# Kernel tuning notes

Measured on AMD Instinct MI355X. Metric: run time of the kernel, lower is better.

The kernel has to match this reference:

```python
import jax, jax.numpy as jnp
import numpy as np

K = 3      # kernel size
P = 1      # padding
HEADS = 6  # num_heads


def setup_inputs() -> dict:
    key = jax.random.key(0)
    ks = jax.random.split(key, 6)
    B, H, W, C = 2, 48, 48, 192
    kk4h = K ** 4 * HEADS  # 486
    sc = 0.02
    return {
        "x": jax.random.normal(ks[0], (B, H, W, C), jnp.float32),
        "v_w": jax.random.normal(ks[1], (C, C), jnp.float32) * sc,
        "attn_w": jax.random.normal(ks[2], (kk4h, C), jnp.float32) * sc,
        "attn_b": jax.random.normal(ks[3], (kk4h,), jnp.float32) * sc,
        "proj_w": jax.random.normal(ks[4], (C, C), jnp.float32) * sc,
        "proj_b": jax.random.normal(ks[5], (C,), jnp.float32) * sc,
    }


def reference(x, v_w, attn_w, attn_b, proj_w, proj_b):
    # OutlookAttention with k=3, s=1 (pool is identity, h=H, w=W), p=1
    B, H, W, C = x.shape
    hd = C // HEADS
    scale = float(hd) ** -0.5

    # value projection (Linear, no bias): [B,H,W,C]
    v = x @ v_w.T

    # unfold: gather kxk neighborhood per pixel, row-major kernel order
    vp = jnp.pad(v, ((0, 0), (P, P), (P, P), (0, 0)))
    patches = jnp.stack(
        [vp[:, ki:ki + H, kj:kj + W, :] for ki in range(K) for kj in range(K)],
        axis=3,
    )  # [B,H,W,k*k,C]
    # -> [B, heads, hw, k*k, hd]
    v_ = patches.reshape(B, H * W, K * K, HEADS, hd).transpose(0, 3, 1, 2, 4)

    # attention logits from (pooled == identity) x: [B,H,W,k^4*heads]
    a = x @ attn_w.T + attn_b
    a = a.reshape(B, H * W, HEADS, K * K, K * K).transpose(0, 2, 1, 3, 4)
    a = jax.nn.softmax(a * scale, axis=-1)  # [B,heads,hw,kk,kk]

    # windowed attention
    out = jnp.einsum("bnlij,bnljd->bnlid", a, v_)  # [B,heads,hw,kk,hd]

    # fold (col2im): scatter-add each kernel tap back, then crop padding
    o = out.transpose(0, 2, 3, 1, 4).reshape(B, H, W, K * K, C)
    acc = jnp.zeros((B, H + 2 * P, W + 2 * P, C), dtype=o.dtype)
    idx = 0
    for ki in range(K):
        for kj in range(K):
            acc = acc.at[:, ki:ki + H, kj:kj + W, :].add(o[:, :, :, idx, :])
            idx += 1
    folded = acc[:, P:P + H, P:P + W, :]

    return folded @ proj_w.T + proj_b
```

## Files before the change

kernel.cpp:

```cpp
#include <hip/hip_runtime.h>

#define BB 2
#define HH 48
#define WW 48
#define CC 192
#define NHEADS 6
#define HD 32
#define KK 9
#define FF 486
#define NPIX (BB*HH*WW)
#define SCALE 0.17677669529663687f

typedef __bf16 bf16;
typedef __attribute__((ext_vector_type(2))) __bf16 bf16x2;
typedef __attribute__((ext_vector_type(4))) __bf16 bf16x4;
typedef __attribute__((ext_vector_type(8))) __bf16 bf16x8;
typedef __attribute__((ext_vector_type(4))) float f32x4;

#define KD 192
#define LDA 200

__global__ __launch_bounds__(256) void gemm_va_kernel(
    const float* __restrict__ x, const float* __restrict__ vw,
    const float* __restrict__ aw, const float* __restrict__ ab,
    bf16* __restrict__ v, float* __restrict__ a)
{
    __shared__ bf16 As[64][LDA];
    __shared__ bf16 Bs[64][LDA];
    const int t = threadIdx.x;
    const int m0 = blockIdx.x * 64;
    const int by = blockIdx.y;
    const bool is_v = (by < 3);
    const int n0 = is_v ? by * 64 : (by - 3) * 64;
    const int Ndim = is_v ? CC : FF;
    const float* W = is_v ? vw : aw;

    #pragma unroll
    for (int i = 0; i < 12; ++i) {
        const int f = t + i * 256;
        const int row = f / 48, c4 = f % 48;
        const float4 xv = *(const float4*)(x + (size_t)(m0 + row) * KD + c4 * 4);
        bf16x4 tv = { (__bf16)xv.x, (__bf16)xv.y, (__bf16)xv.z, (__bf16)xv.w };
        *(bf16x4*)(&As[row][c4 * 4]) = tv;
    }
    #pragma unroll
    for (int i = 0; i < 12; ++i) {
        const int f = t + i * 256;
        const int row = f / 48, c4 = f % 48;
        float4 wv = make_float4(0.f, 0.f, 0.f, 0.f);
        if (n0 + row < Ndim)
            wv = *(const float4*)(W + (size_t)(n0 + row) * KD + c4 * 4);
        bf16x4 tv = { (__bf16)wv.x, (__bf16)wv.y, (__bf16)wv.z, (__bf16)wv.w };
        *(bf16x4*)(&Bs[row][c4 * 4]) = tv;
    }
    __syncthreads();

    const int wave = t >> 6, lane = t & 63;
    const int wm = (wave >> 1) * 32;
    const int wn = (wave & 1) * 32;
    const int lrow = lane & 15;
    const int lk   = (lane >> 4) * 8;

    f32x4 acc[2][2] = {};
    #pragma unroll
    for (int ks = 0; ks < 6; ++ks) {
        bf16x8 afr[2], bfr[2];
        #pragma unroll
        for (int j = 0; j < 2; ++j) {
            afr[j] = *(const bf16x8*)(&As[wm + j * 16 + lrow][ks * 32 + lk]);
            bfr[j] = *(const bf16x8*)(&Bs[wn + j * 16 + lrow][ks * 32 + lk]);
        }
        #pragma unroll
        for (int i = 0; i < 2; ++i)
            #pragma unroll
            for (int j = 0; j < 2; ++j)
                acc[i][j] = __builtin_amdgcn_mfma_f32_16x16x32_bf16(afr[i], bfr[j], acc[i][j], 0, 0, 0);
    }

    const int crow = (lane >> 4) * 4;
    if (is_v) {
        #pragma unroll
        for (int j = 0; j < 2; ++j) {
            const int col = n0 + wn + j * 16 + lrow;
            #pragma unroll
            for (int i = 0; i < 2; ++i)
                #pragma unroll
                for (int r = 0; r < 4; ++r) {
                    const int row = m0 + wm + i * 16 + crow + r;
                    v[(size_t)row * CC + col] = (__bf16)acc[i][j][r];
                }
        }
    } else {
        #pragma unroll
        for (int j = 0; j < 2; ++j) {
            const int col = n0 + wn + j * 16 + lrow;
            if (col < FF) {
                const float bv = ab[col];
                #pragma unroll
                for (int i = 0; i < 2; ++i)
                    #pragma unroll
                    for (int r = 0; r < 4; ++r) {
                        const int row = m0 + wm + i * 16 + crow + r;
                        a[(size_t)row * FF + col] = acc[i][j][r] + bv;
                    }
            }
        }
    }
}

__global__ void attn_kernel(const bf16* __restrict__ v, const float* __restrict__ a,
                            bf16* __restrict__ o) {
    int n = blockIdx.x;
    int tid = threadIdx.x;
    int b = n / (HH * WW), rem = n % (HH * WW), h = rem / WW, w = rem % WW;
    __shared__ float p[FF];
    __shared__ float vl[KK][CC];

    for (int f = tid; f < FF; f += CC) p[f] = a[n * FF + f];
    #pragma unroll
    for (int j = 0; j < KK; ++j) {
        int hh = h + j / 3 - 1, ww = w + j % 3 - 1;
        if (hh >= 0 && hh < HH && ww >= 0 && ww < WW)
            vl[j][tid] = (float)v[((size_t)(b * HH + hh) * WW + ww) * CC + tid];
        else
            vl[j][tid] = 0.f;
    }
    __syncthreads();

    if (tid < NHEADS * KK) {
        float* row = p + tid * KK;
        float t[KK];
        float m = -1e30f;
        #pragma unroll
        for (int j = 0; j < KK; ++j) { t[j] = row[j] * SCALE; m = fmaxf(m, t[j]); }
        float s = 0.f;
        #pragma unroll
        for (int j = 0; j < KK; ++j) { t[j] = __expf(t[j] - m); s += t[j]; }
        float inv = 1.f / s;
        #pragma unroll
        for (int j = 0; j < KK; ++j) row[j] = t[j] * inv;
    }
    __syncthreads();

    int head = tid / HD;
    const float* ph = p + head * 81;
    #pragma unroll
    for (int i = 0; i < KK; ++i) {
        float acc = 0.f;
        #pragma unroll
        for (int j = 0; j < KK; ++j) acc += ph[i * 9 + j] * vl[j][tid];
        o[((size_t)n * KK + i) * CC + tid] = (__bf16)acc;
    }
}

__global__ void fold_kernel(const bf16x2* __restrict__ o, bf16x2* __restrict__ folded) {
    const int idx = blockIdx.x * blockDim.x + threadIdx.x;
    const int c2 = idx % 96, n = idx / 96;
    const int b = n / (HH * WW), rem = n % (HH * WW), y = rem / WW, x = rem % WW;
    float s0 = 0.f, s1 = 0.f;
    #pragma unroll
    for (int ki = 0; ki < 3; ++ki) {
        const int gy = y + 1 - ki;
        if (gy < 0 || gy >= HH) continue;
        #pragma unroll
        for (int kj = 0; kj < 3; ++kj) {
            const int gx = x + 1 - kj;
            if (gx < 0 || gx >= WW) continue;
            const size_t ps = (size_t)(b * HH + gy) * WW + gx;
            const bf16x2 ov = o[(ps * KK + ki * 3 + kj) * 96 + c2];
            s0 += (float)ov.x; s1 += (float)ov.y;
        }
    }
    bf16x2 r = { (__bf16)s0, (__bf16)s1 };
    folded[(size_t)n * 96 + c2] = r;
}

__global__ __launch_bounds__(256) void proj_kernel(
    const bf16* __restrict__ folded, const float* __restrict__ pw,
    const float* __restrict__ pb, float* __restrict__ out)
{
    __shared__ bf16 As[32][LDA];
    __shared__ bf16 Bs[64][LDA];
    const int t = threadIdx.x;
    const int m0 = blockIdx.x * 32;
    const int n0 = blockIdx.y * 64;

    #pragma unroll
    for (int i = 0; i < 3; ++i) {
        const int f = t + i * 256;
        const int row = f / 24, c8 = f % 24;
        const bf16x8 av = *(const bf16x8*)(folded + (size_t)(m0 + row) * KD + c8 * 8);
        *(bf16x8*)(&As[row][c8 * 8]) = av;
    }
    #pragma unroll
    for (int i = 0; i < 12; ++i) {
        const int f = t + i * 256;
        const int row = f / 48, c4 = f % 48;
        const float4 wv = *(const float4*)(pw + (size_t)(n0 + row) * KD + c4 * 4);
        bf16x4 tv = { (__bf16)wv.x, (__bf16)wv.y, (__bf16)wv.z, (__bf16)wv.w };
        *(bf16x4*)(&Bs[row][c4 * 4]) = tv;
    }
    __syncthreads();

    const int wave = t >> 6, lane = t & 63;
    const int wm = (wave & 1) * 16;
    const int wn = (wave >> 1) * 32;
    const int lrow = lane & 15;
    const int lk   = (lane >> 4) * 8;

    f32x4 acc[2] = {};
    #pragma unroll
    for (int ks = 0; ks < 6; ++ks) {
        bf16x8 afr = *(const bf16x8*)(&As[wm + lrow][ks * 32 + lk]);
        #pragma unroll
        for (int j = 0; j < 2; ++j) {
            bf16x8 bfr = *(const bf16x8*)(&Bs[wn + j * 16 + lrow][ks * 32 + lk]);
            acc[j] = __builtin_amdgcn_mfma_f32_16x16x32_bf16(afr, bfr, acc[j], 0, 0, 0);
        }
    }

    const int crow = (lane >> 4) * 4;
    #pragma unroll
    for (int j = 0; j < 2; ++j) {
        const int col = n0 + wn + j * 16 + lrow;
        const float bv = pb[col];
        #pragma unroll
        for (int r = 0; r < 4; ++r) {
            const int row = m0 + wm + crow + r;
            out[(size_t)row * CC + col] = acc[j][r] + bv;
        }
    }
}

extern "C" void kernel_launch(void* const* d_in, const int* in_sizes, int n_in,
                              void* d_out, int out_size, void* d_ws, size_t ws_size,
                              hipStream_t stream) {
    const float* x   = (const float*)d_in[0];
    const float* vw  = (const float*)d_in[1];
    const float* aw  = (const float*)d_in[2];
    const float* ab  = (const float*)d_in[3];
    const float* pw  = (const float*)d_in[4];
    const float* pb  = (const float*)d_in[5];
    float* out = (float*)d_out;

    float* a      = (float*)d_ws;
    bf16* v       = (bf16*)(a + (size_t)NPIX * FF);
    bf16* o       = v + (size_t)NPIX * CC;
    bf16* folded  = o + (size_t)NPIX * KK * CC;

    dim3 blk(256);
    dim3 grid_va(NPIX / 64, 3 + 8);
    dim3 grid_pj(NPIX / 32, CC / 64);

    gemm_va_kernel<<<grid_va, blk, 0, stream>>>(x, vw, aw, ab, v, a);
    attn_kernel<<<NPIX, CC, 0, stream>>>(v, a, o);
    fold_kernel<<<(NPIX * 96) / 256, blk, 0, stream>>>((const bf16x2*)o, (bf16x2*)folded);
    proj_kernel<<<grid_pj, blk, 0, stream>>>(folded, pw, pb, out);
}
```

Measured before the change: 104.5 us.

## Fuse outlook attention with fold by gathering neighbor contributions per output pixel

Replaces the separate attention and fold kernels with one kernel that, per output pixel, loads a 5x5 value window and the attention logits of its 9 neighboring source pixels, recomputes their softmax, and accumulates the folded result directly. This removes the large intermediate per-tap output buffer and a kernel launch. In exchange, each pixel's logits are read and softmaxed nine times and shared memory per block grows, which may lower occupancy.

```diff
diff --git a/kernel.cpp b/kernel.cpp
--- a/kernel.cpp
+++ b/kernel.cpp
@@ -12,7 +12,6 @@
 #define SCALE 0.17677669529663687f
 
 typedef __bf16 bf16;
-typedef __attribute__((ext_vector_type(2))) __bf16 bf16x2;
 typedef __attribute__((ext_vector_type(4))) __bf16 bf16x4;
 typedef __attribute__((ext_vector_type(8))) __bf16 bf16x8;
 typedef __attribute__((ext_vector_type(4))) float f32x4;
@@ -108,27 +107,39 @@
     }
 }
 
-__global__ void attn_kernel(const bf16* __restrict__ v, const float* __restrict__ a,
-                            bf16* __restrict__ o) {
-    int n = blockIdx.x;
-    int tid = threadIdx.x;
-    int b = n / (HH * WW), rem = n % (HH * WW), h = rem / WW, w = rem % WW;
-    __shared__ float p[FF];
-    __shared__ float vl[KK][CC];
-
-    for (int f = tid; f < FF; f += CC) p[f] = a[n * FF + f];
-    #pragma unroll
-    for (int j = 0; j < KK; ++j) {
-        int hh = h + j / 3 - 1, ww = w + j % 3 - 1;
-        if (hh >= 0 && hh < HH && ww >= 0 && ww < WW)
-            vl[j][tid] = (float)v[((size_t)(b * HH + hh) * WW + ww) * CC + tid];
-        else
-            vl[j][tid] = 0.f;
-    }
-    __syncthreads();
-
-    if (tid < NHEADS * KK) {
-        float* row = p + tid * KK;
+__global__ void attn_fold_kernel(const bf16* __restrict__ v,
+                                 const float* __restrict__ a,
+                                 bf16* __restrict__ folded) {
+    const int n = blockIdx.x;
+    const int tid = threadIdx.x;
+    const int b = n / (HH * WW), rem = n % (HH * WW), y = rem / WW, x = rem % WW;
+
+    __shared__ float p[KK][FF];
+    __shared__ float vl[5][5][CC];
+
+    #pragma unroll
+    for (int r = 0; r < 25; ++r) {
+        const int gy = y + r / 5 - 2, gx = x + r % 5 - 2;
+        float val = 0.f;
+        if (gy >= 0 && gy < HH && gx >= 0 && gx < WW)
+            val = (float)v[((size_t)(b * HH + gy) * WW + gx) * CC + tid];
+        vl[r / 5][r % 5][tid] = val;
+    }
+    #pragma unroll
+    for (int i = 0; i < KK; ++i) {
+        const int ny = y + 1 - i / 3, nx = x + 1 - i % 3;
+        if (ny >= 0 && ny < HH && nx >= 0 && nx < WW) {
+            const float* an = a + ((size_t)(b * HH + ny) * WW + nx) * FF;
+            for (int f = tid; f < FF; f += CC) p[i][f] = an[f];
+        }
+    }
+    __syncthreads();
+
+    for (int r = tid; r < KK * 54; r += CC) {
+        const int i = r / 54, hr = r % 54;
+        const int ny = y + 1 - i / 3, nx = x + 1 - i % 3;
+        if (ny < 0 || ny >= HH || nx < 0 || nx >= WW) continue;
+        float* row = &p[i][hr * 9];
         float t[KK];
         float m = -1e30f;
         #pragma unroll
@@ -136,43 +147,25 @@
         float s = 0.f;
         #pragma unroll
         for (int j = 0; j < KK; ++j) { t[j] = __expf(t[j] - m); s += t[j]; }
-        float inv = 1.f / s;
+        const float inv = 1.f / s;
         #pragma unroll
         for (int j = 0; j < KK; ++j) row[j] = t[j] * inv;
     }
     __syncthreads();
 
-    int head = tid / HD;
-    const float* ph = p + head * 81;
+    const int head = tid / HD;
+    float acc = 0.f;
     #pragma unroll
     for (int i = 0; i < KK; ++i) {
-        float acc = 0.f;
-        #pragma unroll
-        for (int j = 0; j < KK; ++j) acc += ph[i * 9 + j] * vl[j][tid];
-        o[((size_t)n * KK + i) * CC + tid] = (__bf16)acc;
-    }
-}
-
-__global__ void fold_kernel(const bf16x2* __restrict__ o, bf16x2* __restrict__ folded) {
-    const int idx = blockIdx.x * blockDim.x + threadIdx.x;
-    const int c2 = idx % 96, n = idx / 96;
-    const int b = n / (HH * WW), rem = n % (HH * WW), y = rem / WW, x = rem % WW;
-    float s0 = 0.f, s1 = 0.f;
-    #pragma unroll
-    for (int ki = 0; ki < 3; ++ki) {
-        const int gy = y + 1 - ki;
-        if (gy < 0 || gy >= HH) continue;
-        #pragma unroll
-        for (int kj = 0; kj < 3; ++kj) {
-            const int gx = x + 1 - kj;
-            if (gx < 0 || gx >= WW) continue;
-            const size_t ps = (size_t)(b * HH + gy) * WW + gx;
-            const bf16x2 ov = o[(ps * KK + ki * 3 + kj) * 96 + c2];
-            s0 += (float)ov.x; s1 += (float)ov.y;
-        }
-    }
-    bf16x2 r = { (__bf16)s0, (__bf16)s1 };
-    folded[(size_t)n * 96 + c2] = r;
+        const int ny = y + 1 - i / 3, nx = x + 1 - i % 3;
+        if (ny < 0 || ny >= HH || nx < 0 || nx >= WW) continue;
+        const float* pn = &p[i][head * 81 + i * 9];
+        const int di = i / 3, dj = i % 3;
+        #pragma unroll
+        for (int j = 0; j < KK; ++j)
+            acc += pn[j] * vl[j / 3 - di + 2][j % 3 - dj + 2][tid];
+    }
+    folded[(size_t)n * CC + tid] = (__bf16)acc;
 }
 
 __global__ __launch_bounds__(256) void proj_kernel(
@@ -245,15 +238,13 @@
 
     float* a      = (float*)d_ws;
     bf16* v       = (bf16*)(a + (size_t)NPIX * FF);
-    bf16* o       = v + (size_t)NPIX * CC;
-    bf16* folded  = o + (size_t)NPIX * KK * CC;
+    bf16* folded  = v + (size_t)NPIX * CC;
 
     dim3 blk(256);
     dim3 grid_va(NPIX / 64, 3 + 8);
     dim3 grid_pj(NPIX / 32, CC / 64);
 
     gemm_va_kernel<<<grid_va, blk, 0, stream>>>(x, vw, aw, ab, v, a);
-    attn_kernel<<<NPIX, CC, 0, stream>>>(v, a, o);
-    fold_kernel<<<(NPIX * 96) / 256, blk, 0, stream>>>((const bf16x2*)o, (bf16x2*)folded);
+    attn_fold_kernel<<<NPIX, CC, 0, stream>>>(v, a, folded);
     proj_kernel<<<grid_pj, blk, 0, stream>>>(folded, pw, pb, out);
 }
```

After: 149.5 us. 1.43x slower.

## Pre-convert inputs and weights to bf16, store logits as bf16, enlarge proj tiles

Applied to the files above, without the earlier changes.

Adds a conversion kernel that turns x and all weight matrices into bf16 once, so the two GEMM kernels load bf16x8 vectors instead of converting fp32 per block. The attention logits intermediate is now stored in bf16, which halves its write and read traffic. The projection GEMM moves from 32x64 to 64x64 tiles with a 2x2 MFMA layout per wave. The cost is an extra kernel launch plus a full read and write of x, and some precision loss in the logits before softmax.

```diff
diff --git a/kernel.cpp b/kernel.cpp
--- a/kernel.cpp
+++ b/kernel.cpp
@@ -20,10 +20,31 @@
 #define KD 192
 #define LDA 200
 
+#define X_F4  221184
+#define VW_F4 9216
+#define AW_F4 23328
+#define PW_F4 9216
+#define TOT_F4 (X_F4 + VW_F4 + AW_F4 + PW_F4)
+
+__global__ void cvt_kernel(const float* __restrict__ x, const float* __restrict__ vw,
+                           const float* __restrict__ aw, const float* __restrict__ pw,
+                           bf16* __restrict__ outb) {
+    const int idx = blockIdx.x * blockDim.x + threadIdx.x;
+    if (idx >= TOT_F4) return;
+    const float* src; int off;
+    if (idx < X_F4)                         { src = x;  off = idx; }
+    else if (idx < X_F4 + VW_F4)            { src = vw; off = idx - X_F4; }
+    else if (idx < X_F4 + VW_F4 + AW_F4)    { src = aw; off = idx - X_F4 - VW_F4; }
+    else                                    { src = pw; off = idx - X_F4 - VW_F4 - AW_F4; }
+    const float4 v4 = *(const float4*)(src + (size_t)off * 4);
+    bf16x4 t = { (__bf16)v4.x, (__bf16)v4.y, (__bf16)v4.z, (__bf16)v4.w };
+    *(bf16x4*)(outb + (size_t)idx * 4) = t;
+}
+
 __global__ __launch_bounds__(256) void gemm_va_kernel(
-    const float* __restrict__ x, const float* __restrict__ vw,
-    const float* __restrict__ aw, const float* __restrict__ ab,
-    bf16* __restrict__ v, float* __restrict__ a)
+    const bf16* __restrict__ xb, const bf16* __restrict__ vwb,
+    const bf16* __restrict__ awb, const float* __restrict__ ab,
+    bf16* __restrict__ v, bf16* __restrict__ a)
 {
     __shared__ bf16 As[64][LDA];
     __shared__ bf16 Bs[64][LDA];
@@ -33,25 +54,25 @@
     const bool is_v = (by < 3);
     const int n0 = is_v ? by * 64 : (by - 3) * 64;
     const int Ndim = is_v ? CC : FF;
-    const float* W = is_v ? vw : aw;
-
-    #pragma unroll
-    for (int i = 0; i < 12; ++i) {
-        const int f = t + i * 256;
-        const int row = f / 48, c4 = f % 48;
-        const float4 xv = *(const float4*)(x + (size_t)(m0 + row) * KD + c4 * 4);
-        bf16x4 tv = { (__bf16)xv.x, (__bf16)xv.y, (__bf16)xv.z, (__bf16)xv.w };
-        *(bf16x4*)(&As[row][c4 * 4]) = tv;
-    }
-    #pragma unroll
-    for (int i = 0; i < 12; ++i) {
-        const int f = t + i * 256;
-        const int row = f / 48, c4 = f % 48;
-        float4 wv = make_float4(0.f, 0.f, 0.f, 0.f);
+    const bf16* W = is_v ? vwb : awb;
+
+    #pragma unroll
+    for (int i = 0; i < 6; ++i) {
+        const int f = t + i * 256;
+        const int row = f / 24, c8 = f % 24;
+        *(bf16x8*)(&As[row][c8 * 8]) =
+            *(const bf16x8*)(xb + (size_t)(m0 + row) * KD + c8 * 8);
+    }
+    #pragma unroll
+    for (int i = 0; i < 6; ++i) {
+        const int f = t + i * 256;
+        const int row = f / 24, c8 = f % 24;
+        bf16x8 wv;
+        #pragma unroll
+        for (int z = 0; z < 8; ++z) wv[z] = (__bf16)0.f;
         if (n0 + row < Ndim)
-            wv = *(const float4*)(W + (size_t)(n0 + row) * KD + c4 * 4);
-        bf16x4 tv = { (__bf16)wv.x, (__bf16)wv.y, (__bf16)wv.z, (__bf16)wv.w };
-        *(bf16x4*)(&Bs[row][c4 * 4]) = tv;
+            wv = *(const bf16x8*)(W + (size_t)(n0 + row) * KD + c8 * 8);
+        *(bf16x8*)(&Bs[row][c8 * 8]) = wv;
     }
     __syncthreads();
 
@@ -101,14 +122,14 @@
                     #pragma unroll
                     for (int r = 0; r < 4; ++r) {
                         const int row = m0 + wm + i * 16 + crow + r;
-                        a[(size_t)row * FF + col] = acc[i][j][r] + bv;
+                        a[(size_t)row * FF + col] = (__bf16)(acc[i][j][r] + bv);
                     }
             }
         }
     }
 }
 
-__global__ void attn_kernel(const bf16* __restrict__ v, const float* __restrict__ a,
+__global__ void attn_kernel(const bf16* __restrict__ v, const bf16* __restrict__ a,
                             bf16* __restrict__ o) {
     int n = blockIdx.x;
     int tid = threadIdx.x;
@@ -116,7 +137,7 @@
     __shared__ float p[FF];
     __shared__ float vl[KK][CC];
 
-    for (int f = tid; f < FF; f += CC) p[f] = a[n * FF + f];
+    for (int f = tid; f < FF; f += CC) p[f] = (float)a[(size_t)n * FF + f];
     #pragma unroll
     for (int j = 0; j < KK; ++j) {
         int hh = h + j / 3 - 1, ww = w + j % 3 - 1;
@@ -176,47 +197,51 @@
 }
 
 __global__ __launch_bounds__(256) void proj_kernel(
-    const bf16* __restrict__ folded, const float* __restrict__ pw,
+    const bf16* __restrict__ folded, const bf16* __restrict__ pwb,
     const float* __restrict__ pb, float* __restrict__ out)
 {
-    __shared__ bf16 As[32][LDA];
+    __shared__ bf16 As[64][LDA];
     __shared__ bf16 Bs[64][LDA];
     const int t = threadIdx.x;
-    const int m0 = blockIdx.x * 32;
+    const int m0 = blockIdx.x * 64;
     const int n0 = blockIdx.y * 64;
 
     #pragma unroll
-    for (int i = 0; i < 3; ++i) {
-        const int f = t + i * 256;
-        const int row = f / 24, c8 = f % 24;
-        const bf16x8 av = *(const bf16x8*)(folded + (size_t)(m0 + row) * KD + c8 * 8);
-        *(bf16x8*)(&As[row][c8 * 8]) = av;
-    }
-    #pragma unroll
-    for (int i = 0; i < 12; ++i) {
-        const int f = t + i * 256;
-        const int row = f / 48, c4 = f % 48;
-        const float4 wv = *(const float4*)(pw + (size_t)(n0 + row) * KD + c4 * 4);
-        bf16x4 tv = { (__bf16)wv.x, (__bf16)wv.y, (__bf16)wv.z, (__bf16)wv.w };
-        *(bf16x4*)(&Bs[row][c4 * 4]) = tv;
+    for (int i = 0; i < 6; ++i) {
+        const int f = t + i * 256;
+        const int row = f / 24, c8 = f % 24;
+        *(bf16x8*)(&As[row][c8 * 8]) =
+            *(const bf16x8*)(folded + (size_t)(m0 + row) * KD + c8 * 8);
+    }
+    #pragma unroll
+    for (int i = 0; i < 6; ++i) {
+        const int f = t + i * 256;
+        const int row = f / 24, c8 = f % 24;
+        *(bf16x8*)(&Bs[row][c8 * 8]) =
+            *(const bf16x8*)(pwb + (size_t)(n0 + row) * KD + c8 * 8);
     }
     __syncthreads();
 
     const int wave = t >> 6, lane = t & 63;
-    const int wm = (wave & 1) * 16;
-    const int wn = (wave >> 1) * 32;
+    const int wm = (wave >> 1) * 32;
+    const int wn = (wave & 1) * 32;
     const int lrow = lane & 15;
     const int lk   = (lane >> 4) * 8;
 
-    f32x4 acc[2] = {};
+    f32x4 acc[2][2] = {};
     #pragma unroll
     for (int ks = 0; ks < 6; ++ks) {
-        bf16x8 afr = *(const bf16x8*)(&As[wm + lrow][ks * 32 + lk]);
-        #pragma unroll
-        for (int j = 0; j < 2; ++j) {
-            bf16x8 bfr = *(const bf16x8*)(&Bs[wn + j * 16 + lrow][ks * 32 + lk]);
-            acc[j] = __builtin_amdgcn_mfma_f32_16x16x32_bf16(afr, bfr, acc[j], 0, 0, 0);
-        }
+        bf16x8 afr[2], bfr[2];
+        #pragma unroll
+        for (int j = 0; j < 2; ++j) {
+            afr[j] = *(const bf16x8*)(&As[wm + j * 16 + lrow][ks * 32 + lk]);
+            bfr[j] = *(const bf16x8*)(&Bs[wn + j * 16 + lrow][ks * 32 + lk]);
+        }
+        #pragma unroll
+        for (int i = 0; i < 2; ++i)
+            #pragma unroll
+            for (int j = 0; j < 2; ++j)
+                acc[i][j] = __builtin_amdgcn_mfma_f32_16x16x32_bf16(afr[i], bfr[j], acc[i][j], 0, 0, 0);
     }
 
     const int crow = (lane >> 4) * 4;
@@ -225,10 +250,12 @@
         const int col = n0 + wn + j * 16 + lrow;
         const float bv = pb[col];
         #pragma unroll
-        for (int r = 0; r < 4; ++r) {
-            const int row = m0 + wm + crow + r;
-            out[(size_t)row * CC + col] = acc[j][r] + bv;
-        }
+        for (int i = 0; i < 2; ++i)
+            #pragma unroll
+            for (int r = 0; r < 4; ++r) {
+                const int row = m0 + wm + i * 16 + crow + r;
+                out[(size_t)row * CC + col] = acc[i][j][r] + bv;
+            }
     }
 }
 
@@ -243,17 +270,23 @@
     const float* pb  = (const float*)d_in[5];
     float* out = (float*)d_out;
 
-    float* a      = (float*)d_ws;
-    bf16* v       = (bf16*)(a + (size_t)NPIX * FF);
-    bf16* o       = v + (size_t)NPIX * CC;
-    bf16* folded  = o + (size_t)NPIX * KK * CC;
+    bf16* a      = (bf16*)d_ws;
+    bf16* o      = a + (size_t)NPIX * FF;
+    bf16* folded = o + (size_t)NPIX * KK * CC;
+    bf16* conv   = folded + (size_t)NPIX * CC;
+    bf16* xb     = conv;
+    bf16* vwb    = conv + 884736;
+    bf16* awb    = vwb + 36864;
+    bf16* pwb    = awb + 93312;
+    bf16* v      = pwb + 36864;
 
     dim3 blk(256);
     dim3 grid_va(NPIX / 64, 3 + 8);
-    dim3 grid_pj(NPIX / 32, CC / 64);
-
-    gemm_va_kernel<<<grid_va, blk, 0, stream>>>(x, vw, aw, ab, v, a);
+    dim3 grid_pj(NPIX / 64, CC / 64);
+
+    cvt_kernel<<<(TOT_F4 + 255) / 256, blk, 0, stream>>>(x, vw, aw, pw, conv);
+    gemm_va_kernel<<<grid_va, blk, 0, stream>>>(xb, vwb, awb, ab, v, a);
     attn_kernel<<<NPIX, CC, 0, stream>>>(v, a, o);
     fold_kernel<<<(NPIX * 96) / 256, blk, 0, stream>>>((const bf16x2*)o, (bf16x2*)folded);
-    proj_kernel<<<grid_pj, blk, 0, stream>>>(folded, pw, pb, out);
-}
+    proj_kernel<<<grid_pj, blk, 0, stream>>>(folded, pwb, pb, out);
+}
```

Result: no change. 102.7 us (-1.6%).
